# Kernel tuning notes

Hardware: AMD Instinct MI355X
Metric: run time of the kernel (lower is better)

The kernel has to match this reference:

```python
import jax, jax.numpy as jnp
import numpy as np

EPS = 1e-5
NEG_SLOPE = 0.2
GN_GROUPS = 8


def conv2d(x, w, b):
    # x: [B,C,H,W], w: [O,I,3,3]
    y = jax.lax.conv_general_dilated(
        x, w, window_strides=(1, 1), padding=((1, 1), (1, 1)),
        dimension_numbers=('NCHW', 'OIHW', 'NCHW'))
    return y + b[None, :, None, None]


def conv3d_d(x, w, b):
    # x: [B,C,D,H,W], w: [O,I,3,1,1] -> conv along D only
    y = jax.lax.conv_general_dilated(
        x, w, window_strides=(1, 1, 1), padding=((1, 1), (0, 0), (0, 0)),
        dimension_numbers=('NCDHW', 'OIDHW', 'NCDHW'))
    return y + b[None, :, None, None, None]


def group_norm(x, gamma, beta):
    # x: [B,C,D,H,W]; normalize per group over (C/g, D, H, W)
    B, C, D, H, W = x.shape
    xg = x.reshape(B, GN_GROUPS, C // GN_GROUPS, D, H, W)
    mu = jnp.mean(xg, axis=(2, 3, 4, 5), keepdims=True)
    var = jnp.var(xg, axis=(2, 3, 4, 5), keepdims=True)
    xn = ((xg - mu) * jax.lax.rsqrt(var + EPS)).reshape(B, C, D, H, W)
    return xn * gamma[None, :, None, None, None] + beta[None, :, None, None, None]


def setup_inputs() -> dict:
    key = jax.random.key(0)
    ks = jax.random.split(key, 8)
    C = 32
    B, D, H, W = 2, 24, 160, 160
    s = lambda fan: 1.0 / np.sqrt(fan)
    return {
        'x': jax.random.normal(ks[0], (B, C, D, H, W), jnp.float32),
        'w_f1': jax.random.normal(ks[1], (2 * C, C, 3, 1, 1), jnp.float32) * s(C * 3),
        'b_f1': jnp.zeros((2 * C,), jnp.float32),
        'gn_g': jnp.ones((2 * C,), jnp.float32),
        'gn_b': jnp.zeros((2 * C,), jnp.float32),
        'w_f2': jax.random.normal(ks[2], (C, 2 * C, 3, 1, 1), jnp.float32) * s(2 * C * 3),
        'b_f2': jnp.zeros((C,), jnp.float32),
        'w_u': jax.random.normal(ks[3], (C, 2 * C, 3, 3), jnp.float32) * s(2 * C * 9),
        'b_u': jnp.zeros((C,), jnp.float32),
        'w_r': jax.random.normal(ks[4], (C, 2 * C, 3, 3), jnp.float32) * s(2 * C * 9),
        'b_r': jnp.zeros((C,), jnp.float32),
        'w_o': jax.random.normal(ks[5], (C, 2 * C, 3, 3), jnp.float32) * s(2 * C * 9),
        'b_o': jnp.zeros((C,), jnp.float32),
    }


def reference(x, w_f1, b_f1, gn_g, gn_b, w_f2, b_f2, w_u, b_u, w_r, b_r, w_o, b_o):
    B, C, D, H, W = x.shape

    # slice_flow: Conv3d(C->2C,(3,1,1)) -> GroupNorm(8) -> LeakyReLU(0.2) -> Conv3d(2C->C,(3,1,1))
    sf = conv3d_d(x, w_f1, b_f1)
    sf = group_norm(sf, gn_g, gn_b)
    sf = jnp.where(sf >= 0, sf, NEG_SLOPE * sf)
    slice_features = conv3d_d(sf, w_f2, b_f2)

    def gru_step(h, xd):
        combined = jnp.concatenate([xd, h], axis=1)
        update = jax.nn.sigmoid(conv2d(combined, w_u, b_u))
        reset = jax.nn.sigmoid(conv2d(combined, w_r, b_r))
        combined_reset = jnp.concatenate([xd, reset * h], axis=1)
        cand = jnp.tanh(conv2d(combined_reset, w_o, b_o))
        h_new = (1.0 - update) * h + update * cand
        return h_new, h_new

    xd = jnp.moveaxis(x, 2, 0)  # [D,B,C,H,W]
    h0 = jnp.zeros((B, C, H, W), x.dtype)
    _, fwd = jax.lax.scan(gru_step, h0, xd)                 # [D,B,C,H,W]
    _, bwd = jax.lax.scan(gru_step, h0, xd, reverse=True)   # aligned with xd order

    enhanced = xd + fwd + bwd                                # [D,B,C,H,W]
    return jnp.moveaxis(enhanced, 0, 2) + slice_features
```

## Files before the change

kernel.cpp:

```cpp
#include <hip/hip_runtime.h>
#include <hip/hip_bf16.h>
#include <stdint.h>

#define EPS_GN 1e-5f
#define NEG_SLOPE 0.2f

static constexpr int  Bn   = 2;
static constexpr int  Cn   = 32;
static constexpr int  Dn   = 24;
static constexpr int  Hn   = 160;
static constexpr int  Wn   = 160;
static constexpr int  HWn  = Hn * Wn;
static constexpr long DHWn = (long)Dn * HWn;
static constexpr long NPIX = (long)Bn * Dn * HWn;

using frag8  = __attribute__((ext_vector_type(8)))  short;
using accf16 = __attribute__((ext_vector_type(16))) float;

__device__ __forceinline__ float bf2f(__hip_bfloat16 v) { return __bfloat162float(v); }
__device__ __forceinline__ __hip_bfloat16 f2bf(float v) { return __float2bfloat16(v); }
__device__ __forceinline__ float sigm(float v) { return 1.f / (1.f + __expf(-v)); }
__device__ __forceinline__ float tanh_(float v) {
    float e = __expf(2.f * v);
    return 1.f - 2.f / (e + 1.f);
}

__global__ __launch_bounds__(256) void bpack1_kernel(
    const float* __restrict__ w, __hip_bfloat16* __restrict__ dst)
{
    int t = blockIdx.x * 256 + threadIdx.x;
    if (t >= 6 * 2 * 64 * 8) return;
    int j    = t & 7;
    int lane = (t >> 3) & 63;
    int idx  = t >> 9;
    int nt   = idx & 1;
    int kb   = idx >> 1;
    int o    = nt * 32 + (lane & 31);
    int k    = kb * 16 + (lane >> 5) * 8 + j;
    int ci   = k & 31;
    int kd   = k >> 5;
    dst[t] = f2bf(w[(o * 32 + ci) * 3 + kd]);
}

__global__ __launch_bounds__(256) void bpack2_kernel(
    const float* __restrict__ w, __hip_bfloat16* __restrict__ dst)
{
    int t = blockIdx.x * 256 + threadIdx.x;
    if (t >= 12 * 64 * 8) return;
    int j    = t & 7;
    int lane = (t >> 3) & 63;
    int kb   = t >> 9;
    int o    = lane & 31;
    int k    = kb * 16 + (lane >> 5) * 8 + j;
    int ci   = k & 63;
    int kd   = k >> 6;
    dst[t] = f2bf(w[(o * 64 + ci) * 3 + kd]);
}

__global__ __launch_bounds__(256) void bpack_kernel(
    const float* __restrict__ w, __hip_bfloat16* __restrict__ dst)
{
    int t = blockIdx.x * 256 + threadIdx.x;
    if (t >= 9 * 4 * 64 * 8) return;
    int j    = t & 7;
    int lane = (t >> 3) & 63;
    int kb   = (t >> 9) & 3;
    int tap  = t >> 11;
    int ci   = kb * 16 + (lane >> 5) * 8 + j;
    int o    = lane & 31;
    dst[t] = f2bf(w[(o * 64 + ci) * 9 + tap]);
}

__global__ __launch_bounds__(256) void tohwc_kernel(
    const float* __restrict__ x, __hip_bfloat16* __restrict__ xhwc)
{
    __shared__ float tile[32][65];
    int bd = blockIdx.y;
    int b  = bd / Dn, d = bd % Dn;
    int p0 = blockIdx.x * 64;
    const float* xb = x + (long)b * Cn * DHWn + (long)d * HWn + p0;
    for (int e = threadIdx.x; e < 2048; e += 256) {
        int c = e >> 6, p = e & 63;
        tile[c][p] = xb[(long)c * DHWn + p];
    }
    __syncthreads();
    __hip_bfloat16* ob = xhwc + ((long)bd * HWn + p0) * 32;
    for (int e = threadIdx.x; e < 2048; e += 256) {
        int p = e >> 5, c = e & 31;
        ob[p * 32 + c] = f2bf(tile[c][p]);
    }
}

__global__ __launch_bounds__(256) void conv1_mfma(
    const __hip_bfloat16* __restrict__ xhwc,
    const __hip_bfloat16* __restrict__ Bp1,
    const float* __restrict__ b1,
    int b,
    __hip_bfloat16* __restrict__ A,
    float* __restrict__ gsum, float* __restrict__ gsq)
{
    int wave = threadIdx.x >> 6;
    int lane = threadIdx.x & 63;
    int ml   = lane & 31;
    int kh   = lane >> 5;
    int bid  = blockIdx.x;
    int sw   = (bid & 7) * 300 + (bid >> 3);
    int tile0 = sw * 8 + wave * 2;

    frag8 bf[6][2];
#pragma unroll
    for (int kb = 0; kb < 6; kb++)
#pragma unroll
        for (int nt = 0; nt < 2; nt++)
            bf[kb][nt] = *(const frag8*)(Bp1 + ((kb * 2 + nt) * 64 + lane) * 8);

    int d  = tile0 / 800;
    int p0 = (tile0 % 800) * 32;

    accf16 acc[2][2];
#pragma unroll
    for (int t = 0; t < 2; t++)
#pragma unroll
        for (int nt = 0; nt < 2; nt++)
#pragma unroll
            for (int i = 0; i < 16; i++) acc[t][nt][i] = 0.f;

    for (int kd = 0; kd < 3; kd++) {
        int dd = d + kd - 1;
        bool valid = (unsigned)dd < (unsigned)Dn;
        const __hip_bfloat16* rp = xhwc + ((long)(b * Dn + dd) * HWn) * 32;
#pragma unroll
        for (int h2 = 0; h2 < 2; h2++) {
            int kb = kd * 2 + h2;
#pragma unroll
            for (int t = 0; t < 2; t++) {
                frag8 a = {};
                if (valid)
                    a = *(const frag8*)(rp + (long)(p0 + t * 32 + ml) * 32 + h2 * 16 + kh * 8);
                acc[t][0] = __builtin_amdgcn_mfma_f32_32x32x16_bf16(a, bf[kb][0], acc[t][0], 0, 0, 0);
                acc[t][1] = __builtin_amdgcn_mfma_f32_32x32x16_bf16(a, bf[kb][1], acc[t][1], 0, 0, 0);
            }
        }
    }

    float bias[2] = { b1[ml], b1[32 + ml] };
    float s[2] = {0.f, 0.f}, q[2] = {0.f, 0.f};
    __hip_bfloat16* Ap = A + (long)d * HWn * 64;
#pragma unroll
    for (int t = 0; t < 2; t++) {
        int pb = p0 + t * 32;
#pragma unroll
        for (int nt = 0; nt < 2; nt++) {
#pragma unroll
            for (int i = 0; i < 16; i++) {
                int row = (i & 3) + 8 * (i >> 2) + 4 * kh;
                float v = acc[t][nt][i] + bias[nt];
                Ap[(long)(pb + row) * 64 + nt * 32 + ml] = f2bf(v);
                s[nt] += v;
                q[nt] += v * v;
            }
        }
    }
#pragma unroll
    for (int nt = 0; nt < 2; nt++) {
        s[nt] += __shfl_xor(s[nt], 32);
        q[nt] += __shfl_xor(q[nt], 32);
    }
    __shared__ float ss[64], sq[64];
    if (threadIdx.x < 64) { ss[threadIdx.x] = 0.f; sq[threadIdx.x] = 0.f; }
    __syncthreads();
    if (lane < 32) {
        atomicAdd(&ss[ml],      s[0]); atomicAdd(&sq[ml],      q[0]);
        atomicAdd(&ss[32 + ml], s[1]); atomicAdd(&sq[32 + ml], q[1]);
    }
    __syncthreads();
    if (threadIdx.x < 64) {
        atomicAdd(&gsum[b * 64 + threadIdx.x], ss[threadIdx.x]);
        atomicAdd(&gsq [b * 64 + threadIdx.x], sq[threadIdx.x]);
    }
}

__global__ __launch_bounds__(64) void finalize_kernel(
    const float* __restrict__ gsum, const float* __restrict__ gsq,
    const float* __restrict__ gn_g, const float* __restrict__ gn_b,
    float* __restrict__ scal, float* __restrict__ shft, int b)
{
    int ci = threadIdx.x;
    if (ci >= 64) return;
    int g = ci >> 3;
    float s = 0.f, qq = 0.f;
#pragma unroll
    for (int k = 0; k < 8; k++) {
        s  += gsum[b * 64 + g * 8 + k];
        qq += gsq [b * 64 + g * 8 + k];
    }
    float N   = 8.0f * (float)DHWn;
    float mu  = s / N;
    float var = qq / N - mu * mu;
    float rs  = rsqrtf(var + EPS_GN);
    float scv = rs * gn_g[ci];
    scal[b * 64 + ci] = scv;
    shft[b * 64 + ci] = gn_b[ci] - mu * scv;
}

__global__ __launch_bounds__(256) void act_kernel(
    __hip_bfloat16* __restrict__ A,
    const float* __restrict__ scal, const float* __restrict__ shft, int b)
{
    __shared__ float sc[64], sh[64];
    if (threadIdx.x < 64) {
        sc[threadIdx.x] = scal[b * 64 + threadIdx.x];
        sh[threadIdx.x] = shft[b * 64 + threadIdx.x];
    }
    __syncthreads();
    long i0 = ((long)blockIdx.x * 256 + threadIdx.x) * 8;
    __hip_bfloat16 loc[8];
    *(frag8*)loc = *(const frag8*)(A + i0);
    int c0 = (int)(i0 & 63);
#pragma unroll
    for (int j = 0; j < 8; j++) {
        float f  = bf2f(loc[j]);
        float an = fmaf(f, sc[c0 + j], sh[c0 + j]);
        loc[j]   = f2bf(fmaxf(an, NEG_SLOPE * an));
    }
    *(frag8*)(A + i0) = *(frag8*)loc;
}

__global__ __launch_bounds__(256) void conv2_mfma(
    const __hip_bfloat16* __restrict__ Aact,
    const __hip_bfloat16* __restrict__ Bp2,
    const float* __restrict__ b2,
    const float* __restrict__ x,
    float* __restrict__ out,
    int b)
{
    int wave = threadIdx.x >> 6;
    int lane = threadIdx.x & 63;
    int ml   = lane & 31;
    int kh   = lane >> 5;
    int bid  = blockIdx.x;
    int sw   = (bid & 7) * 600 + (bid >> 3);
    int tile = sw * 4 + wave;

    frag8 bf[12];
#pragma unroll
    for (int kb = 0; kb < 12; kb++)
        bf[kb] = *(const frag8*)(Bp2 + (kb * 64 + lane) * 8);

    int d  = tile / 800;
    int p0 = (tile % 800) * 32;

    accf16 acc;
#pragma unroll
    for (int i = 0; i < 16; i++) acc[i] = 0.f;

    for (int kd = 0; kd < 3; kd++) {
        int dd = d + kd - 1;
        bool valid = (unsigned)dd < (unsigned)Dn;
        const __hip_bfloat16* rp = Aact + (long)dd * HWn * 64;
#pragma unroll
        for (int qq = 0; qq < 4; qq++) {
            frag8 a = {};
            if (valid)
                a = *(const frag8*)(rp + (long)(p0 + ml) * 64 + qq * 16 + kh * 8);
            acc = __builtin_amdgcn_mfma_f32_32x32x16_bf16(a, bf[kd * 4 + qq], acc, 0, 0, 0);
        }
    }

    __shared__ float tb[4][32][33];
    float bias = b2[ml];
    const float* xb = x   + (long)b * Cn * DHWn + (long)d * HWn;
    float*       ob = out + (long)b * Cn * DHWn + (long)d * HWn;
#pragma unroll
    for (int i = 0; i < 16; i++) {
        int row = (i & 3) + 8 * (i >> 2) + 4 * kh;
        tb[wave][row][ml] = acc[i] + bias;
    }
#pragma unroll
    for (int r2 = 0; r2 < 16; r2++) {
        int c = r2 * 2 + kh;
        float v = tb[wave][ml][c] + xb[(long)c * DHWn + p0 + ml];
        ob[(long)c * DHWn + p0 + ml] = v;
    }
}

__global__ __launch_bounds__(256) void gru_step_mfma(
    const __hip_bfloat16* __restrict__ xhwc,
    int dfwd, int dbwd,
    const __hip_bfloat16* __restrict__ hold,
    const __hip_bfloat16* __restrict__ Bu,
    const __hip_bfloat16* __restrict__ Br,
    const __hip_bfloat16* __restrict__ Bo,
    const float* __restrict__ bu, const float* __restrict__ br,
    const float* __restrict__ bo,
    __hip_bfloat16* __restrict__ hnew,
    float* __restrict__ out)
{
    int db   = blockIdx.y;
    int dir  = db >> 1, b = db & 1;
    int d    = dir ? dbwd : dfwd;
    int wave = threadIdx.x >> 6;
    int lane = threadIdx.x & 63;
    int ml   = lane & 31;
    int kh   = lane >> 5;

    int bidx = blockIdx.x;
    int sw   = (bidx & 7) * 25 + (bidx >> 3);
    int tile = sw * 4 + wave;
    int trow = tile / 20, tcol = tile % 20;
    int py0  = trow * 4,  px0  = tcol * 8;

    __shared__ __hip_bfloat16 rhl[4][64][40];
    __shared__ float tb[4][32][33];

    const __hip_bfloat16* xb  = xhwc + ((long)b * Dn + d) * HWn * 32;
    const __hip_bfloat16* hb  = hold + (long)db * HWn * 32;
    __hip_bfloat16*       hnb = hnew + (long)db * HWn * 32;

    float bias_r = br[ml], bias_u = bu[ml], bias_o = bo[ml];

    {
        int hr0 = ml / 10,        hc0 = ml - hr0 * 10;
        int hp1 = 32 + ml;
        int hr1 = hp1 / 10,       hc1 = hp1 - hr1 * 10;
        int hy[2] = { py0 - 1 + hr0, py0 - 1 + hr1 };
        int hx[2] = { px0 - 1 + hc0, px0 - 1 + hc1 };

        accf16 ar[2];
#pragma unroll
        for (int t = 0; t < 2; t++)
#pragma unroll
            for (int i = 0; i < 16; i++) ar[t][i] = 0.f;

        for (int tap = 0; tap < 9; tap++) {
            int dy = tap / 3 - 1, dx = tap % 3 - 1;
            bool ok[2]; long poff[2];
#pragma unroll
            for (int t = 0; t < 2; t++) {
                int yy = hy[t] + dy, xx = hx[t] + dx;
                ok[t]   = ((unsigned)yy < (unsigned)Hn) & ((unsigned)xx < (unsigned)Wn);
                poff[t] = ((long)(yy * Wn + xx)) * 32;
            }
#pragma unroll
            for (int kb = 0; kb < 4; kb++) {
                frag8 brf = *(const frag8*)(Br + ((tap * 4 + kb) * 64 + lane) * 8);
                int ch = kb * 16 + kh * 8;
                const __hip_bfloat16* bsel = (kb < 2) ? (xb + ch) : (hb + (ch - 32));
#pragma unroll
                for (int t = 0; t < 2; t++) {
                    frag8 a = {};
                    if (ok[t]) a = *(const frag8*)(bsel + poff[t]);
                    ar[t] = __builtin_amdgcn_mfma_f32_32x32x16_bf16(a, brf, ar[t], 0, 0, 0);
                }
            }
        }
#pragma unroll
        for (int t = 0; t < 2; t++) {
#pragma unroll
            for (int i = 0; i < 16; i++) {
                int row = (i & 3) + 8 * (i >> 2) + 4 * kh;
                int hp2 = t * 32 + row;
                int hr  = hp2 / 10, hc = hp2 - hr * 10;
                int hy2 = py0 - 1 + hr, hx2 = px0 - 1 + hc;
                bool v  = ((unsigned)hy2 < (unsigned)Hn) & ((unsigned)hx2 < (unsigned)Wn);
                float hpv = v ? bf2f(hb[((long)(hy2 * Wn + hx2)) * 32 + ml]) : 0.f;
                rhl[wave][hp2][ml] = f2bf(sigm(ar[t][i] + bias_r) * hpv);
            }
        }
    }

    {
        int prow = ml >> 3, pcol = ml & 7;
        int oy = py0 + prow, ox = px0 + pcol;

        accf16 au, ao;
#pragma unroll
        for (int i = 0; i < 16; i++) { au[i] = 0.f; ao[i] = 0.f; }

        for (int tap = 0; tap < 9; tap++) {
            int dy = tap / 3 - 1, dx = tap % 3 - 1;
            int yy = oy + dy, xx = ox + dx;
            bool ok  = ((unsigned)yy < (unsigned)Hn) & ((unsigned)xx < (unsigned)Wn);
            long poff = ((long)(yy * Wn + xx)) * 32;
            int hp = (prow + 1 + dy) * 10 + (pcol + 1 + dx);
#pragma unroll
            for (int kb = 0; kb < 4; kb++) {
                frag8 buf = *(const frag8*)(Bu + ((tap * 4 + kb) * 64 + lane) * 8);
                frag8 bof = *(const frag8*)(Bo + ((tap * 4 + kb) * 64 + lane) * 8);
                int ch = kb * 16 + kh * 8;
                if (kb < 2) {
                    frag8 a = {};
                    if (ok) a = *(const frag8*)(xb + ch + poff);
                    au = __builtin_amdgcn_mfma_f32_32x32x16_bf16(a, buf, au, 0, 0, 0);
                    ao = __builtin_amdgcn_mfma_f32_32x32x16_bf16(a, bof, ao, 0, 0, 0);
                } else {
                    frag8 ah = {};
                    if (ok) ah = *(const frag8*)(hb + (ch - 32) + poff);
                    au = __builtin_amdgcn_mfma_f32_32x32x16_bf16(ah, buf, au, 0, 0, 0);
                    frag8 arh = *(const frag8*)(&rhl[wave][hp][(kb - 2) * 16 + kh * 8]);
                    ao = __builtin_amdgcn_mfma_f32_32x32x16_bf16(arh, bof, ao, 0, 0, 0);
                }
            }
        }

        float* ob = out + (long)b * Cn * DHWn + (long)d * HWn;
#pragma unroll
        for (int i = 0; i < 16; i++) {
            int lp  = (i & 3) + 8 * (i >> 2) + 4 * kh;
            int pyy = py0 + (lp >> 3), pxx = px0 + (lp & 7);
            long pix = (long)pyy * Wn + pxx;
            float uu  = sigm(au[i] + bias_u);
            float cc  = tanh_(ao[i] + bias_o);
            float hpv = bf2f(hb[pix * 32 + ml]);
            float hn  = (1.f - uu) * hpv + uu * cc;
            hnb[pix * 32 + ml] = f2bf(hn);
            tb[wave][lp][ml] = hn;
        }
        int pyy = py0 + (ml >> 3), pxx = px0 + (ml & 7);
        long pix = (long)pyy * Wn + pxx;
#pragma unroll
        for (int r2 = 0; r2 < 16; r2++) {
            int c = r2 * 2 + kh;
            ob[(long)c * DHWn + pix] += tb[wave][ml][c];
        }
    }
}

extern "C" void kernel_launch(void* const* d_in, const int* in_sizes, int n_in,
                              void* d_out, int out_size, void* d_ws, size_t ws_size,
                              hipStream_t stream)
{
    const float* x    = (const float*)d_in[0];
    const float* w_f1 = (const float*)d_in[1];
    const float* b_f1 = (const float*)d_in[2];
    const float* gn_g = (const float*)d_in[3];
    const float* gn_b = (const float*)d_in[4];
    const float* w_f2 = (const float*)d_in[5];
    const float* b_f2 = (const float*)d_in[6];
    const float* w_u  = (const float*)d_in[7];
    const float* b_u  = (const float*)d_in[8];
    const float* w_r  = (const float*)d_in[9];
    const float* b_r  = (const float*)d_in[10];
    const float* w_o  = (const float*)d_in[11];
    const float* b_o  = (const float*)d_in[12];
    float* out = (float*)d_out;

    char* ws = (char*)d_ws;
    __hip_bfloat16* Bp1 = (__hip_bfloat16*)ws;
    __hip_bfloat16* Bp2 = Bp1 + 6144;
    __hip_bfloat16* Bu  = Bp2 + 6144;
    __hip_bfloat16* Br  = Bu + 18432;
    __hip_bfloat16* Bo  = Br + 18432;
    float* gsum = (float*)(Bo + 18432);
    float* gsq  = gsum + 128;
    float* scal = gsq + 128;
    float* shft = scal + 128;
    char* big = (char*)(shft + 128);
    big = (char*)(((uintptr_t)big + 255) & ~(uintptr_t)255);

    __hip_bfloat16* xhwc = (__hip_bfloat16*)big;
    __hip_bfloat16* Apre = (__hip_bfloat16*)(big + 78643200L);
    __hip_bfloat16* hA   = (__hip_bfloat16*)(big + 78643200L);
    __hip_bfloat16* hB   = (__hip_bfloat16*)(big + 85196800L);

    size_t need = (size_t)(big - ws) + 157286400UL;
    if (ws_size < need) return;

    bpack1_kernel<<<24, 256, 0, stream>>>(w_f1, Bp1);
    bpack2_kernel<<<24, 256, 0, stream>>>(w_f2, Bp2);
    bpack_kernel<<<72, 256, 0, stream>>>(w_u, Bu);
    bpack_kernel<<<72, 256, 0, stream>>>(w_r, Br);
    bpack_kernel<<<72, 256, 0, stream>>>(w_o, Bo);
    hipMemsetAsync(gsum, 0, 256 * sizeof(float), stream);

    tohwc_kernel<<<dim3(400, Bn * Dn), 256, 0, stream>>>(x, xhwc);

    for (int b = 0; b < Bn; b++) {
        conv1_mfma<<<2400, 256, 0, stream>>>(xhwc, Bp1, b_f1, b, Apre, gsum, gsq);
        finalize_kernel<<<1, 64, 0, stream>>>(gsum, gsq, gn_g, gn_b, scal, shft, b);
        act_kernel<<<19200, 256, 0, stream>>>(Apre, scal, shft, b);
        conv2_mfma<<<4800, 256, 0, stream>>>(Apre, Bp2, b_f2, x, out, b);
    }

    hipMemsetAsync(hA, 0, 6553600, stream);
    __hip_bfloat16* hbufs[2] = { hA, hB };
    for (int s = 0; s < Dn; s++) {
        int dfwd = s, dbwd = Dn - 1 - s;
        __hip_bfloat16* hold = hbufs[s & 1];
        __hip_bfloat16* hnew = hbufs[(s + 1) & 1];
        gru_step_mfma<<<dim3(200, 4), 256, 0, stream>>>(
            xhwc, dfwd, dbwd, hold, Bu, Br, Bo, b_u, b_r, b_o, hnew, out);
    }
}
```

Measured before the change: 2.017 ms.

## Precompute input-side GRU gate convolutions for all slices before the recurrence

Adds a batched kernel that computes the x-half of the update, reset and candidate convolutions for every slice at once and stores them as bf16. The per-step GRU kernel then does only the h-half convolutions, using an LDS-staged h tile with a wider halo, and reads the precomputed gate inputs. The goal is to take half of the MFMA work off the serial 24-step chain and run it in one fully parallel launch. The cost is roughly 235 MB of extra workspace and more global traffic. A fallback keeps the old path when the workspace is too small, so whether the new path runs depends on the workspace size.

```diff
diff --git a/kernel.cpp b/kernel.cpp
--- a/kernel.cpp
+++ b/kernel.cpp
@@ -284,6 +284,233 @@
     }
 }
 
+__global__ __launch_bounds__(256) void gx3_mfma(
+    const __hip_bfloat16* __restrict__ xhwc,
+    const __hip_bfloat16* __restrict__ Bu,
+    const __hip_bfloat16* __restrict__ Br,
+    const __hip_bfloat16* __restrict__ Bo,
+    const float* __restrict__ bu, const float* __restrict__ br,
+    const float* __restrict__ bo,
+    __hip_bfloat16* __restrict__ gxr,
+    __hip_bfloat16* __restrict__ gxu,
+    __hip_bfloat16* __restrict__ gxo)
+{
+    int wave = threadIdx.x >> 6;
+    int lane = threadIdx.x & 63;
+    int ml   = lane & 31;
+    int kh   = lane >> 5;
+    int bid  = blockIdx.x;
+    int sw   = (bid & 7) * 600 + (bid >> 3);
+    int tile0 = sw * 8 + wave * 2;
+
+    int bslice = tile0 / (Dn * 800);
+    int rem    = tile0 - bslice * (Dn * 800);
+    int d      = rem / 800;
+    int p0     = (rem - d * 800) * 32;
+
+    const __hip_bfloat16* xb = xhwc + ((long)(bslice * Dn + d) * HWn) * 32;
+
+    int pyt[2], pxt[2];
+#pragma unroll
+    for (int t = 0; t < 2; t++) {
+        int pb = p0 + t * 32;
+        pyt[t] = pb / Wn;
+        pxt[t] = pb % Wn;
+    }
+
+    accf16 ar[2], au[2], ao[2];
+#pragma unroll
+    for (int t = 0; t < 2; t++)
+#pragma unroll
+        for (int i = 0; i < 16; i++) { ar[t][i] = 0.f; au[t][i] = 0.f; ao[t][i] = 0.f; }
+
+    for (int tap = 0; tap < 9; tap++) {
+        int dy = tap / 3 - 1, dx = tap % 3 - 1;
+        bool ok[2]; long poff[2];
+#pragma unroll
+        for (int t = 0; t < 2; t++) {
+            int yy = pyt[t] + dy, xx = pxt[t] + ml + dx;
+            ok[t]   = ((unsigned)yy < (unsigned)Hn) & ((unsigned)xx < (unsigned)Wn);
+            poff[t] = ((long)(yy * Wn + xx)) * 32;
+        }
+#pragma unroll
+        for (int kbh = 0; kbh < 2; kbh++) {
+            frag8 brf = *(const frag8*)(Br + ((tap * 4 + kbh) * 64 + lane) * 8);
+            frag8 buf = *(const frag8*)(Bu + ((tap * 4 + kbh) * 64 + lane) * 8);
+            frag8 bof = *(const frag8*)(Bo + ((tap * 4 + kbh) * 64 + lane) * 8);
+            int ch = kbh * 16 + kh * 8;
+#pragma unroll
+            for (int t = 0; t < 2; t++) {
+                frag8 a = {};
+                if (ok[t]) a = *(const frag8*)(xb + poff[t] + ch);
+                ar[t] = __builtin_amdgcn_mfma_f32_32x32x16_bf16(a, brf, ar[t], 0, 0, 0);
+                au[t] = __builtin_amdgcn_mfma_f32_32x32x16_bf16(a, buf, au[t], 0, 0, 0);
+                ao[t] = __builtin_amdgcn_mfma_f32_32x32x16_bf16(a, bof, ao[t], 0, 0, 0);
+            }
+        }
+    }
+
+    float biasr = br[ml], biasu = bu[ml], biaso = bo[ml];
+    long base = (long)(bslice * Dn + d) * HWn;
+#pragma unroll
+    for (int t = 0; t < 2; t++) {
+        int pb = p0 + t * 32;
+#pragma unroll
+        for (int i = 0; i < 16; i++) {
+            int row = (i & 3) + 8 * (i >> 2) + 4 * kh;
+            long off = (base + pb + row) * 32 + ml;
+            gxr[off] = f2bf(ar[t][i] + biasr);
+            gxu[off] = f2bf(au[t][i] + biasu);
+            gxo[off] = f2bf(ao[t][i] + biaso);
+        }
+    }
+}
+
+__global__ __launch_bounds__(256) void gru_step2_mfma(
+    int dfwd, int dbwd,
+    const __hip_bfloat16* __restrict__ hold,
+    __hip_bfloat16* __restrict__ hnew,
+    const __hip_bfloat16* __restrict__ gxr,
+    const __hip_bfloat16* __restrict__ gxu,
+    const __hip_bfloat16* __restrict__ gxo,
+    const __hip_bfloat16* __restrict__ Bu,
+    const __hip_bfloat16* __restrict__ Br,
+    const __hip_bfloat16* __restrict__ Bo,
+    float* __restrict__ out)
+{
+    int db   = blockIdx.y;
+    int dir  = db >> 1, b = db & 1;
+    int d    = dir ? dbwd : dfwd;
+    int wave = threadIdx.x >> 6;
+    int lane = threadIdx.x & 63;
+    int ml   = lane & 31;
+    int kh   = lane >> 5;
+
+    int bidx = blockIdx.x;
+    int sw   = (bidx & 7) * 25 + (bidx >> 3);
+    int prow = sw / 10, pcol = sw % 10;
+    int py0  = prow * 8, px0 = pcol * 16;
+
+    __shared__ __hip_bfloat16 hs[256][40];
+    __shared__ __hip_bfloat16 rhl[184][40];
+    __shared__ float tb[4][32][33];
+
+    const __hip_bfloat16* hb  = hold + (long)db * HWn * 32;
+    __hip_bfloat16*       hnb = hnew + (long)db * HWn * 32;
+    long gbase = (long)(b * Dn + d) * HWn;
+    const __hip_bfloat16* gxr_s = gxr + gbase * 32;
+    const __hip_bfloat16* gxu_s = gxu + gbase * 32;
+    const __hip_bfloat16* gxo_s = gxo + gbase * 32;
+
+    {
+        int tid = threadIdx.x;
+        for (int e = tid; e < 960; e += 256) {
+            int sp  = e >> 2, cid = e & 3;
+            int sr  = sp / 20, sc2 = sp - sr * 20;
+            int gy  = py0 - 2 + sr, gx2 = px0 - 2 + sc2;
+            frag8 v = {};
+            if (((unsigned)gy < (unsigned)Hn) & ((unsigned)gx2 < (unsigned)Wn))
+                v = *(const frag8*)(hb + ((long)(gy * Wn + gx2)) * 32 + cid * 8);
+            *(frag8*)(&hs[sp][cid * 8]) = v;
+        }
+        if (tid < 64) {
+            int sp = 240 + (tid >> 2), cid = tid & 3;
+            frag8 z = {};
+            *(frag8*)(&hs[sp][cid * 8]) = z;
+        }
+    }
+    __syncthreads();
+
+#pragma unroll
+    for (int tt = 0; tt < 2; tt++) {
+        if (tt == 0 || wave < 2) {
+            int tile = tt ? (4 + wave) : wave;
+            int hp1 = tile * 32 + ml;
+            int hr1 = hp1 / 18, hc1 = hp1 - hr1 * 18;
+            int s0  = (hr1 + 1) * 20 + (hc1 + 1);
+
+            accf16 ar;
+#pragma unroll
+            for (int i = 0; i < 16; i++) ar[i] = 0.f;
+
+            for (int tap = 0; tap < 9; tap++) {
+                int dy = tap / 3 - 1, dx = tap % 3 - 1;
+                int sidx = s0 + dy * 20 + dx;
+#pragma unroll
+                for (int kbh = 0; kbh < 2; kbh++) {
+                    frag8 brf = *(const frag8*)(Br + ((tap * 4 + 2 + kbh) * 64 + lane) * 8);
+                    frag8 a = *(const frag8*)(&hs[sidx][kbh * 16 + kh * 8]);
+                    ar = __builtin_amdgcn_mfma_f32_32x32x16_bf16(a, brf, ar, 0, 0, 0);
+                }
+            }
+#pragma unroll
+            for (int i = 0; i < 16; i++) {
+                int row = (i & 3) + 8 * (i >> 2) + 4 * kh;
+                int hp = tile * 32 + row;
+                if (hp < 180) {
+                    int hr = hp / 18, hc = hp - hr * 18;
+                    int gy = py0 - 1 + hr, gx2 = px0 - 1 + hc;
+                    float g = 0.f;
+                    if (((unsigned)gy < (unsigned)Hn) & ((unsigned)gx2 < (unsigned)Wn))
+                        g = bf2f(gxr_s[((long)(gy * Wn + gx2)) * 32 + ml]);
+                    float hval = bf2f(hs[(hr + 1) * 20 + (hc + 1)][ml]);
+                    rhl[hp][ml] = f2bf(sigm(ar[i] + g) * hval);
+                }
+            }
+        }
+    }
+    __syncthreads();
+
+    {
+        int wr = wave >> 1, wc = wave & 1;
+        int blr = wr * 4 + (ml >> 3);
+        int blc = wc * 8 + (ml & 7);
+
+        accf16 au, ao;
+#pragma unroll
+        for (int i = 0; i < 16; i++) { au[i] = 0.f; ao[i] = 0.f; }
+
+        for (int tap = 0; tap < 9; tap++) {
+            int dy = tap / 3 - 1, dx = tap % 3 - 1;
+            int su = (blr + 2 + dy) * 20 + (blc + 2 + dx);
+            int sc2 = (blr + 1 + dy) * 18 + (blc + 1 + dx);
+#pragma unroll
+            for (int kbh = 0; kbh < 2; kbh++) {
+                frag8 buf = *(const frag8*)(Bu + ((tap * 4 + 2 + kbh) * 64 + lane) * 8);
+                frag8 bof = *(const frag8*)(Bo + ((tap * 4 + 2 + kbh) * 64 + lane) * 8);
+                frag8 ah  = *(const frag8*)(&hs[su][kbh * 16 + kh * 8]);
+                frag8 arh = *(const frag8*)(&rhl[sc2][kbh * 16 + kh * 8]);
+                au = __builtin_amdgcn_mfma_f32_32x32x16_bf16(ah,  buf, au, 0, 0, 0);
+                ao = __builtin_amdgcn_mfma_f32_32x32x16_bf16(arh, bof, ao, 0, 0, 0);
+            }
+        }
+
+        float* ob = out + (long)b * Cn * DHWn + (long)d * HWn;
+#pragma unroll
+        for (int i = 0; i < 16; i++) {
+            int lp = (i & 3) + 8 * (i >> 2) + 4 * kh;
+            int pr = lp >> 3, pc = lp & 7;
+            int gy = py0 + wr * 4 + pr, gx2 = px0 + wc * 8 + pc;
+            long pix = (long)gy * Wn + gx2;
+            float gu = bf2f(gxu_s[pix * 32 + ml]);
+            float go = bf2f(gxo_s[pix * 32 + ml]);
+            float uu = sigm(au[i] + gu);
+            float cc = tanh_(ao[i] + go);
+            float hval = bf2f(hs[(wr * 4 + pr + 2) * 20 + (wc * 8 + pc + 2)][ml]);
+            float hn = (1.f - uu) * hval + uu * cc;
+            hnb[pix * 32 + ml] = f2bf(hn);
+            tb[wave][lp][ml] = hn;
+        }
+        int gy2 = py0 + wr * 4 + (ml >> 3), gx3_ = px0 + wc * 8 + (ml & 7);
+        long pix2 = (long)gy2 * Wn + gx3_;
+#pragma unroll
+        for (int r2 = 0; r2 < 16; r2++) {
+            int c = r2 * 2 + kh;
+            ob[(long)c * DHWn + pix2] += tb[wave][ml][c];
+        }
+    }
+}
+
 __global__ __launch_bounds__(256) void gru_step_mfma(
     const __hip_bfloat16* __restrict__ xhwc,
     int dfwd, int dbwd,
@@ -370,8 +597,8 @@
     }
 
     {
-        int prow = ml >> 3, pcol = ml & 7;
-        int oy = py0 + prow, ox = px0 + pcol;
+        int prow2 = ml >> 3, pcol2 = ml & 7;
+        int oy = py0 + prow2, ox = px0 + pcol2;
 
         accf16 au, ao;
 #pragma unroll
@@ -382,7 +609,7 @@
             int yy = oy + dy, xx = ox + dx;
             bool ok  = ((unsigned)yy < (unsigned)Hn) & ((unsigned)xx < (unsigned)Wn);
             long poff = ((long)(yy * Wn + xx)) * 32;
-            int hp = (prow + 1 + dy) * 10 + (pcol + 1 + dx);
+            int hp = (prow2 + 1 + dy) * 10 + (pcol2 + 1 + dx);
 #pragma unroll
             for (int kb = 0; kb < 4; kb++) {
                 frag8 buf = *(const frag8*)(Bu + ((tap * 4 + kb) * 64 + lane) * 8);
@@ -458,13 +685,22 @@
     char* big = (char*)(shft + 128);
     big = (char*)(((uintptr_t)big + 255) & ~(uintptr_t)255);
 
+    const long SL = 78643200L;
     __hip_bfloat16* xhwc = (__hip_bfloat16*)big;
-    __hip_bfloat16* Apre = (__hip_bfloat16*)(big + 78643200L);
-    __hip_bfloat16* hA   = (__hip_bfloat16*)(big + 78643200L);
-    __hip_bfloat16* hB   = (__hip_bfloat16*)(big + 85196800L);
-
-    size_t need = (size_t)(big - ws) + 157286400UL;
-    if (ws_size < need) return;
+    __hip_bfloat16* Apre = (__hip_bfloat16*)(big + SL);
+    __hip_bfloat16* gxr  = (__hip_bfloat16*)(big + SL);
+    __hip_bfloat16* gxu  = (__hip_bfloat16*)(big + 2 * SL);
+    __hip_bfloat16* gxo  = (__hip_bfloat16*)(big + 3 * SL);
+    __hip_bfloat16* hA_b = (__hip_bfloat16*)(big + 4 * SL);
+    __hip_bfloat16* hB_b = (__hip_bfloat16*)(big + 4 * SL + 6553600L);
+    __hip_bfloat16* hA_s = (__hip_bfloat16*)(big + SL);
+    __hip_bfloat16* hB_s = (__hip_bfloat16*)(big + SL + 6553600L);
+
+    size_t base_off   = (size_t)(big - ws);
+    size_t need_small = base_off + 2 * (size_t)SL;
+    size_t need_big   = base_off + 4 * (size_t)SL + 2 * 6553600UL;
+    if (ws_size < need_small) return;
+    bool big_path = (ws_size >= need_big);
 
     bpack1_kernel<<<24, 256, 0, stream>>>(w_f1, Bp1);
     bpack2_kernel<<<24, 256, 0, stream>>>(w_f2, Bp2);
@@ -482,13 +718,25 @@
         conv2_mfma<<<4800, 256, 0, stream>>>(Apre, Bp2, b_f2, x, out, b);
     }
 
-    hipMemsetAsync(hA, 0, 6553600, stream);
-    __hip_bfloat16* hbufs[2] = { hA, hB };
-    for (int s = 0; s < Dn; s++) {
-        int dfwd = s, dbwd = Dn - 1 - s;
-        __hip_bfloat16* hold = hbufs[s & 1];
-        __hip_bfloat16* hnew = hbufs[(s + 1) & 1];
-        gru_step_mfma<<<dim3(200, 4), 256, 0, stream>>>(
-            xhwc, dfwd, dbwd, hold, Bu, Br, Bo, b_u, b_r, b_o, hnew, out);
-    }
-}
+    if (big_path) {
+        gx3_mfma<<<4800, 256, 0, stream>>>(xhwc, Bu, Br, Bo, b_u, b_r, b_o,
+                                           gxr, gxu, gxo);
+        hipMemsetAsync(hA_b, 0, 6553600, stream);
+        __hip_bfloat16* hbufs[2] = { hA_b, hB_b };
+        for (int s = 0; s < Dn; s++) {
+            int dfwd = s, dbwd = Dn - 1 - s;
+            gru_step2_mfma<<<dim3(200, 4), 256, 0, stream>>>(
+                dfwd, dbwd, hbufs[s & 1], hbufs[(s + 1) & 1],
+                gxr, gxu, gxo, Bu, Br, Bo, out);
+        }
+    } else {
+        hipMemsetAsync(hA_s, 0, 6553600, stream);
+        __hip_bfloat16* hbufs[2] = { hA_s, hB_s };
+        for (int s = 0; s < Dn; s++) {
+            int dfwd = s, dbwd = Dn - 1 - s;
+            gru_step_mfma<<<dim3(200, 4), 256, 0, stream>>>(
+                xhwc, dfwd, dbwd, hbufs[s & 1], Bu, Br, Bo,
+                b_u, b_r, b_o, hbufs[(s + 1) & 1], out);
+        }
+    }
+}
```

Result: slower. 2.152 ms (+6.7%).
